# Optimization experiments

Measured on AMD Instinct MI355X. Metric: run time of the kernel, lower is better.

The kernel has to match this reference:

```python
import jax, jax.numpy as jnp
import numpy as np

NUM_CLASSES = 10
OUTPUT_DIM = 128
HIDDEN_DIM = 64


def setup_inputs() -> dict:
    key = jax.random.key(0)
    k1, k2, k3, k4, k5, k6 = jax.random.split(key, 6)
    B, S, F = 16, 4096, 512
    X_support = jax.random.normal(k1, (B, S, F), dtype=jnp.float32)
    y_support = jax.random.randint(k2, (B, S), 0, NUM_CLASSES, dtype=jnp.int32)
    # MLP params: Linear(6, HIDDEN) -> GELU -> Linear(HIDDEN, OUTPUT)
    w1 = jax.random.normal(k3, (6, HIDDEN_DIM), dtype=jnp.float32) * (1.0 / np.sqrt(6.0))
    b1 = jax.random.normal(k4, (HIDDEN_DIM,), dtype=jnp.float32) * 0.01
    w2 = jax.random.normal(k5, (HIDDEN_DIM, OUTPUT_DIM), dtype=jnp.float32) * (1.0 / np.sqrt(HIDDEN_DIM))
    b2 = jax.random.normal(k6, (OUTPUT_DIM,), dtype=jnp.float32) * 0.01
    return {"X_support": X_support, "y_support": y_support,
            "w1": w1, "b1": b1, "w2": w2, "b2": b2}


def _feature_target_stats(X, y):
    """Vectorized equivalent of FeatureTargetStatsEncoder per-(batch,feature) loops.
    X: [B, S, F] float, y: [B, S] int class labels. Returns stats [B, F, 6]."""
    B, S, F = X.shape
    missing_rate = jnp.isnan(X).astype(X.dtype).mean(axis=1)           # [B, F]
    Xc = jnp.nan_to_num(X, nan=0.0)
    gmean = Xc.mean(axis=1)                                            # [B, F]
    variance = Xc.var(axis=1)                                          # biased (unbiased=False)
    absX = jnp.abs(Xc)
    mean_abs = absX.mean(axis=1)
    max_abs = absX.max(axis=1)
    # unique_ratio: count distinct values per (b, f) via sort + diff
    xs = jnp.sort(Xc, axis=1)
    n_unique = 1.0 + (jnp.diff(xs, axis=1) != 0).astype(Xc.dtype).sum(axis=1)
    unique_ratio = n_unique / S
    # classification target score: between-class variance / overall variance
    onehot = jax.nn.one_hot(y, NUM_CLASSES, dtype=Xc.dtype)            # [B, S, C]
    counts = onehot.sum(axis=1)                                        # [B, C]
    csum = jnp.einsum('bsc,bsf->bcf', onehot, Xc)                      # [B, C, F]
    cmean = csum / jnp.maximum(counts, 1.0)[:, :, None]
    dev2 = (cmean - gmean[:, None, :]) ** 2
    between = (counts[:, :, None] * dev2).sum(axis=1) / jnp.maximum(counts.sum(axis=1), 1.0)[:, None]
    target_score = between / jnp.maximum(variance, 1e-6)
    stats = jnp.stack([target_score, missing_rate, unique_ratio,
                       variance, mean_abs, max_abs], axis=-1)          # [B, F, 6]
    return jnp.nan_to_num(stats, nan=0.0, posinf=0.0, neginf=0.0)


def reference(X_support, y_support, w1, b1, w2, b2):
    stats = _feature_target_stats(X_support, y_support)                # [B, F, 6]
    h = jax.nn.gelu(stats @ w1 + b1, approximate=False)               # exact GELU like nn.GELU()
    return h @ w2 + b2                                                 # [B, F, OUTPUT_DIM]
```

## Files before the change

kernel.cpp:

```cpp
#include <hip/hip_runtime.h>
#include <math.h>

#define NS 4096
#define NF 512
#define NB 16
#define NC 10
#define HSIZE 8192
#define HMASK 8191
#define HEMPTY 0xFFFFFFFFu
#define WS_XT_OFF 1024

__global__ void count_classes_kernel(const int* __restrict__ y, float* __restrict__ counts) {
    __shared__ int hist[NC];
    const int b = blockIdx.x;
    if (threadIdx.x < NC) hist[threadIdx.x] = 0;
    __syncthreads();
    for (int s = threadIdx.x; s < NS; s += blockDim.x)
        atomicAdd(&hist[y[b * NS + s]], 1);
    __syncthreads();
    if (threadIdx.x < NC) counts[b * NC + threadIdx.x] = (float)hist[threadIdx.x];
}

__device__ __forceinline__ float wave_reduce_add(float v) {
    #pragma unroll
    for (int off = 32; off > 0; off >>= 1) v += __shfl_down(v, off, 64);
    return v;
}
__device__ __forceinline__ float wave_reduce_max(float v) {
    #pragma unroll
    for (int off = 32; off > 0; off >>= 1) v = fmaxf(v, __shfl_down(v, off, 64));
    return v;
}

__launch_bounds__(256)
__global__ void transpose_kernel(const float* __restrict__ X, float* __restrict__ XT) {
    __shared__ float t[64][65];
    const int b  = blockIdx.x;
    const int s0 = blockIdx.y * 64;
    const int f0 = blockIdx.z * 64;
    const int tid = threadIdx.x;

    const int fi = (tid & 15) * 4;
    const int si = tid >> 4;
    const float* Xb = X + ((size_t)b * NS + s0) * NF + f0;
    #pragma unroll
    for (int i = 0; i < 4; i++) {
        const int s = si + 16 * i;
        const float4 v = *(const float4*)(Xb + (size_t)s * NF + fi);
        t[s][fi + 0] = v.x; t[s][fi + 1] = v.y;
        t[s][fi + 2] = v.z; t[s][fi + 3] = v.w;
    }
    __syncthreads();

    const int sj = (tid & 15) * 4;
    const int fj = tid >> 4;
    float* XTb = XT + ((size_t)b * NF + f0) * NS + s0;
    #pragma unroll
    for (int i = 0; i < 4; i++) {
        const int f = fj + 16 * i;
        float4 v;
        v.x = t[sj + 0][f]; v.y = t[sj + 1][f];
        v.z = t[sj + 2][f]; v.w = t[sj + 3][f];
        *(float4*)(XTb + (size_t)f * NS + sj) = v;
    }
}

__launch_bounds__(256)
__global__ void fused_stats_mlp_xt(const float* __restrict__ XT,
                                   const int* __restrict__ y,
                                   const float* __restrict__ counts,
                                   const float* __restrict__ w1,
                                   const float* __restrict__ b1,
                                   const float* __restrict__ w2,
                                   const float* __restrict__ b2,
                                   float* __restrict__ out) {
    __shared__ unsigned int hash[HSIZE];
    __shared__ float red[4][16];
    __shared__ float stats_s[6];
    __shared__ float h_s[64];

    const int w = blockIdx.x;
    const int g = (w & 7) * 1024 + (w >> 3);
    const int b = g >> 9;
    const int f = g & (NF - 1);
    const int tid = threadIdx.x;

    #pragma unroll
    for (int i = 0; i < HSIZE / 256; i++) hash[tid + i * 256] = HEMPTY;
    __syncthreads();

    const float4* Xc4 = (const float4*)(XT + ((size_t)b * NF + f) * NS);
    const int4*   yp4 = (const int4*)(y + (size_t)b * NS);

    float sum = 0.f, sumsq = 0.f, sumabs = 0.f, maxabs = 0.f, nancnt = 0.f, uniq = 0.f;
    float csum[NC];
    #pragma unroll
    for (int c = 0; c < NC; c++) csum[c] = 0.f;

    float4 xv[4]; int4 yv[4];
    #pragma unroll
    for (int k = 0; k < 4; k++) {
        xv[k] = Xc4[k * 256 + tid];
        yv[k] = yp4[k * 256 + tid];
    }

    #pragma unroll
    for (int k = 0; k < 4; k++) {
        const float xe[4] = { xv[k].x, xv[k].y, xv[k].z, xv[k].w };
        const int   ye[4] = { yv[k].x, yv[k].y, yv[k].z, yv[k].w };
        #pragma unroll
        for (int j = 0; j < 4; j++) {
            float x = xe[j];
            if (x != x) { nancnt += 1.f; x = 0.f; }
            sum += x;
            sumsq = fmaf(x, x, sumsq);
            const float a = fabsf(x);
            sumabs += a;
            maxabs = fmaxf(maxabs, a);
            const int yc = ye[j];
            #pragma unroll
            for (int c = 0; c < NC; c++) csum[c] += (yc == c) ? x : 0.f;
            unsigned int pat = __float_as_uint(x);
            if (pat == 0x80000000u) pat = 0u;
            unsigned int slot = (pat * 2654435761u) >> 19;
            for (;;) {
                const unsigned int old = atomicCAS(&hash[slot], HEMPTY, pat);
                if (old == HEMPTY) { uniq += 1.f; break; }
                if (old == pat) break;
                slot = (slot + 1) & HMASK;
            }
        }
    }

    sum    = wave_reduce_add(sum);
    sumsq  = wave_reduce_add(sumsq);
    sumabs = wave_reduce_add(sumabs);
    nancnt = wave_reduce_add(nancnt);
    uniq   = wave_reduce_add(uniq);
    maxabs = wave_reduce_max(maxabs);
    #pragma unroll
    for (int c = 0; c < NC; c++) csum[c] = wave_reduce_add(csum[c]);

    const int wave = tid >> 6, lane = tid & 63;
    if (lane == 0) {
        red[wave][0] = sum;    red[wave][1] = sumsq; red[wave][2] = sumabs;
        red[wave][3] = nancnt; red[wave][4] = uniq;  red[wave][5] = maxabs;
        #pragma unroll
        for (int c = 0; c < NC; c++) red[wave][6 + c] = csum[c];
    }
    __syncthreads();

    if (tid == 0) {
        float t[16];
        #pragma unroll
        for (int v = 0; v < 16; v++) t[v] = red[0][v];
        #pragma unroll
        for (int wv = 1; wv < 4; wv++) {
            #pragma unroll
            for (int v = 0; v < 16; v++) {
                if (v == 5) t[v] = fmaxf(t[v], red[wv][v]);
                else        t[v] += red[wv][v];
            }
        }
        const float invS = 1.f / (float)NS;
        const float gmean    = t[0] * invS;
        const float variance = fmaxf(t[1] * invS - gmean * gmean, 0.f);
        const float mean_abs = t[2] * invS;
        const float missing  = t[3] * invS;
        const float n_unique = t[4];
        const float max_abs  = t[5];
        float between = 0.f;
        #pragma unroll
        for (int c = 0; c < NC; c++) {
            const float cnt = counts[b * NC + c];
            const float cm  = t[6 + c] / fmaxf(cnt, 1.f);
            const float d   = cm - gmean;
            between += cnt * d * d;
        }
        between *= invS;
        const float target = between / fmaxf(variance, 1e-6f);
        float st[6] = { target, missing, n_unique * invS, variance, mean_abs, max_abs };
        #pragma unroll
        for (int i = 0; i < 6; i++) {
            float v = st[i];
            if (!(fabsf(v) < INFINITY)) v = 0.f;
            stats_s[i] = v;
        }
    }
    __syncthreads();

    if (tid < 64) {
        float z = b1[tid];
        #pragma unroll
        for (int i = 0; i < 6; i++) z = fmaf(stats_s[i], w1[i * 64 + tid], z);
        h_s[tid] = 0.5f * z * (1.f + erff(z * 0.70710678118654752440f));
    }
    __syncthreads();
    if (tid < 128) {
        float o = b2[tid];
        #pragma unroll
        for (int j = 0; j < 64; j++) o = fmaf(h_s[j], w2[j * 128 + tid], o);
        out[(size_t)g * 128 + tid] = o;
    }
}

__launch_bounds__(256)
__global__ void fused_stats_mlp_kernel(const float* __restrict__ X,
                                       const int* __restrict__ y,
                                       const float* __restrict__ counts,
                                       const float* __restrict__ w1,
                                       const float* __restrict__ b1,
                                       const float* __restrict__ w2,
                                       const float* __restrict__ b2,
                                       float* __restrict__ out) {
    __shared__ unsigned int hash[HSIZE];
    __shared__ float red[4][16];
    __shared__ float stats_s[6];
    __shared__ float h_s[64];

    const int w = blockIdx.x;
    const int g = (w & 7) * 1024 + (w >> 3);
    const int b = g >> 9;
    const int f = g & (NF - 1);
    const int tid = threadIdx.x;

    #pragma unroll
    for (int i = 0; i < HSIZE / 256; i++) hash[tid + i * 256] = HEMPTY;
    __syncthreads();

    const float* Xp = X + (size_t)b * NS * NF + f;
    const int*   yp = y + b * NS;

    float sum = 0.f, sumsq = 0.f, sumabs = 0.f, maxabs = 0.f, nancnt = 0.f, uniq = 0.f;
    float csum[NC];
    #pragma unroll
    for (int c = 0; c < NC; c++) csum[c] = 0.f;

    #pragma unroll
    for (int k0 = 0; k0 < 16; k0 += 8) {
        float xv[8]; int yv[8];
        #pragma unroll
        for (int k = 0; k < 8; k++) {
            const int s = (k0 + k) * 256 + tid;
            xv[k] = Xp[(size_t)s * NF];
            yv[k] = yp[s];
        }
        #pragma unroll
        for (int k = 0; k < 8; k++) {
            float x = xv[k];
            if (x != x) { nancnt += 1.f; x = 0.f; }
            sum += x;
            sumsq = fmaf(x, x, sumsq);
            const float a = fabsf(x);
            sumabs += a;
            maxabs = fmaxf(maxabs, a);
            const int yc = yv[k];
            #pragma unroll
            for (int c = 0; c < NC; c++) csum[c] += (yc == c) ? x : 0.f;
            unsigned int pat = __float_as_uint(x);
            if (pat == 0x80000000u) pat = 0u;
            unsigned int slot = (pat * 2654435761u) >> 19;
            for (;;) {
                const unsigned int old = atomicCAS(&hash[slot], HEMPTY, pat);
                if (old == HEMPTY) { uniq += 1.f; break; }
                if (old == pat) break;
                slot = (slot + 1) & HMASK;
            }
        }
    }

    sum    = wave_reduce_add(sum);
    sumsq  = wave_reduce_add(sumsq);
    sumabs = wave_reduce_add(sumabs);
    nancnt = wave_reduce_add(nancnt);
    uniq   = wave_reduce_add(uniq);
    maxabs = wave_reduce_max(maxabs);
    #pragma unroll
    for (int c = 0; c < NC; c++) csum[c] = wave_reduce_add(csum[c]);

    const int wave = tid >> 6, lane = tid & 63;
    if (lane == 0) {
        red[wave][0] = sum;    red[wave][1] = sumsq; red[wave][2] = sumabs;
        red[wave][3] = nancnt; red[wave][4] = uniq;  red[wave][5] = maxabs;
        #pragma unroll
        for (int c = 0; c < NC; c++) red[wave][6 + c] = csum[c];
    }
    __syncthreads();

    if (tid == 0) {
        float t[16];
        #pragma unroll
        for (int v = 0; v < 16; v++) t[v] = red[0][v];
        #pragma unroll
        for (int wv = 1; wv < 4; wv++) {
            #pragma unroll
            for (int v = 0; v < 16; v++) {
                if (v == 5) t[v] = fmaxf(t[v], red[wv][v]);
                else        t[v] += red[wv][v];
            }
        }
        const float invS = 1.f / (float)NS;
        const float gmean    = t[0] * invS;
        const float variance = fmaxf(t[1] * invS - gmean * gmean, 0.f);
        const float mean_abs = t[2] * invS;
        const float missing  = t[3] * invS;
        const float n_unique = t[4];
        const float max_abs  = t[5];
        float between = 0.f;
        #pragma unroll
        for (int c = 0; c < NC; c++) {
            const float cnt = counts[b * NC + c];
            const float cm  = t[6 + c] / fmaxf(cnt, 1.f);
            const float d   = cm - gmean;
            between += cnt * d * d;
        }
        between *= invS;
        const float target = between / fmaxf(variance, 1e-6f);
        float st[6] = { target, missing, n_unique * invS, variance, mean_abs, max_abs };
        #pragma unroll
        for (int i = 0; i < 6; i++) {
            float v = st[i];
            if (!(fabsf(v) < INFINITY)) v = 0.f;
            stats_s[i] = v;
        }
    }
    __syncthreads();

    if (tid < 64) {
        float z = b1[tid];
        #pragma unroll
        for (int i = 0; i < 6; i++) z = fmaf(stats_s[i], w1[i * 64 + tid], z);
        h_s[tid] = 0.5f * z * (1.f + erff(z * 0.70710678118654752440f));
    }
    __syncthreads();
    if (tid < 128) {
        float o = b2[tid];
        #pragma unroll
        for (int j = 0; j < 64; j++) o = fmaf(h_s[j], w2[j * 128 + tid], o);
        out[(size_t)g * 128 + tid] = o;
    }
}

extern "C" void kernel_launch(void* const* d_in, const int* in_sizes, int n_in,
                              void* d_out, int out_size, void* d_ws, size_t ws_size,
                              hipStream_t stream) {
    const float* X  = (const float*)d_in[0];
    const int*   y  = (const int*)d_in[1];
    const float* w1 = (const float*)d_in[2];
    const float* b1 = (const float*)d_in[3];
    const float* w2 = (const float*)d_in[4];
    const float* b2 = (const float*)d_in[5];
    float* out    = (float*)d_out;
    float* counts = (float*)d_ws;

    count_classes_kernel<<<NB, 256, 0, stream>>>(y, counts);

    const size_t xt_bytes = (size_t)NB * NF * NS * sizeof(float);
    if (ws_size >= xt_bytes + WS_XT_OFF) {
        float* XT = (float*)((char*)d_ws + WS_XT_OFF);
        transpose_kernel<<<dim3(NB, NS / 64, NF / 64), 256, 0, stream>>>(X, XT);
        fused_stats_mlp_xt<<<NB * NF, 256, 0, stream>>>(XT, y, counts, w1, b1, w2, b2, out);
    } else {
        fused_stats_mlp_kernel<<<NB * NF, 256, 0, stream>>>(X, y, counts, w1, b1, w2, b2, out);
    }
}
```

Before: 378.1 us.

## Software-pipeline hash-set CAS inserts and fold class counting into transpose

The unique-count hash insertion is split into a batched first CAS and a deferred collision-resolution step, interleaved with prefetch of the next X/y chunk so that LDS atomic latency overlaps with loads and arithmetic. The class histogram moves into the transpose kernel's first blocks, which removes one kernel launch. Reduction scratch now reuses the hash LDS buffer to cut shared memory, the hash reset uses vectorized stores, and launch bounds request 5 blocks per CU. This costs more registers, and the extra syncthreads inside a conditional branch of the transpose is uniform per block, so it is safe.

After: 388.5 us. 1.03x slower.

```diff
diff --git a/kernel.cpp b/kernel.cpp
--- a/kernel.cpp
+++ b/kernel.cpp
@@ -33,8 +33,10 @@
 }
 
 __launch_bounds__(256)
-__global__ void transpose_kernel(const float* __restrict__ X, float* __restrict__ XT) {
+__global__ void transpose_kernel(const float* __restrict__ X, float* __restrict__ XT,
+                                 const int* __restrict__ y, float* __restrict__ counts) {
     __shared__ float t[64][65];
+    __shared__ int hist[NC];
     const int b  = blockIdx.x;
     const int s0 = blockIdx.y * 64;
     const int f0 = blockIdx.z * 64;
@@ -63,9 +65,73 @@
         v.z = t[sj + 2][f]; v.w = t[sj + 3][f];
         *(float4*)(XTb + (size_t)f * NS + sj) = v;
     }
-}
-
-__launch_bounds__(256)
+
+    if (blockIdx.y == 0 && blockIdx.z == 0) {
+        if (tid < NC) hist[tid] = 0;
+        __syncthreads();
+        const int4* yb = (const int4*)(y + (size_t)b * NS);
+        #pragma unroll
+        for (int i = 0; i < 4; i++) {
+            const int4 v = yb[i * 256 + tid];
+            atomicAdd(&hist[v.x], 1); atomicAdd(&hist[v.y], 1);
+            atomicAdd(&hist[v.z], 1); atomicAdd(&hist[v.w], 1);
+        }
+        __syncthreads();
+        if (tid < NC) counts[b * NC + tid] = (float)hist[tid];
+    }
+}
+
+__device__ __forceinline__ void prep_group(const float4 xf, const int4 yi,
+    float& sum, float& sumsq, float& sumabs, float& maxabs, float& nancnt,
+    float* csum, unsigned int* P, unsigned int* S)
+{
+    const float xe[4] = { xf.x, xf.y, xf.z, xf.w };
+    const int   ye[4] = { yi.x, yi.y, yi.z, yi.w };
+    #pragma unroll
+    for (int j = 0; j < 4; j++) {
+        float x = xe[j];
+        if (x != x) { nancnt += 1.f; x = 0.f; }
+        sum += x;
+        sumsq = fmaf(x, x, sumsq);
+        const float a = fabsf(x);
+        sumabs += a;
+        maxabs = fmaxf(maxabs, a);
+        #pragma unroll
+        for (int c = 0; c < NC; c++) csum[c] += (ye[j] == c) ? x : 0.f;
+        unsigned int p = __float_as_uint(x);
+        if (p == 0x80000000u) p = 0u;
+        P[j] = p;
+        S[j] = (p * 2654435761u) >> 19;
+    }
+}
+
+__device__ __forceinline__ void cas_batch(unsigned int* hash,
+    const unsigned int* S, const unsigned int* P, unsigned int* O)
+{
+    #pragma unroll
+    for (int j = 0; j < 4; j++)
+        O[j] = atomicCAS(&hash[S[j]], HEMPTY, P[j]);
+}
+
+__device__ __forceinline__ void resolve_batch(unsigned int* hash,
+    const unsigned int* S, const unsigned int* P, const unsigned int* O, float& uniq)
+{
+    #pragma unroll
+    for (int j = 0; j < 4; j++) {
+        const unsigned int o = O[j];
+        if (o == HEMPTY) { uniq += 1.f; continue; }
+        if (o == P[j]) continue;
+        unsigned int sl = S[j];
+        for (;;) {
+            sl = (sl + 1) & HMASK;
+            const unsigned int oo = atomicCAS(&hash[sl], HEMPTY, P[j]);
+            if (oo == HEMPTY) { uniq += 1.f; break; }
+            if (oo == P[j]) break;
+        }
+    }
+}
+
+__launch_bounds__(256, 5)
 __global__ void fused_stats_mlp_xt(const float* __restrict__ XT,
                                    const int* __restrict__ y,
                                    const float* __restrict__ counts,
@@ -74,19 +140,19 @@
                                    const float* __restrict__ w2,
                                    const float* __restrict__ b2,
                                    float* __restrict__ out) {
-    __shared__ unsigned int hash[HSIZE];
-    __shared__ float red[4][16];
-    __shared__ float stats_s[6];
-    __shared__ float h_s[64];
+    __shared__ __align__(16) unsigned int hash[HSIZE];
 
     const int w = blockIdx.x;
     const int g = (w & 7) * 1024 + (w >> 3);
     const int b = g >> 9;
     const int f = g & (NF - 1);
     const int tid = threadIdx.x;
-
-    #pragma unroll
-    for (int i = 0; i < HSIZE / 256; i++) hash[tid + i * 256] = HEMPTY;
+    const int wave = tid >> 6, lane = tid & 63;
+
+    uint4* h4 = (uint4*)hash;
+    const uint4 e4 = make_uint4(HEMPTY, HEMPTY, HEMPTY, HEMPTY);
+    #pragma unroll
+    for (int i = 0; i < HSIZE / 4 / 256; i++) h4[i * 256 + tid] = e4;
     __syncthreads();
 
     const float4* Xc4 = (const float4*)(XT + ((size_t)b * NF + f) * NS);
@@ -97,40 +163,34 @@
     #pragma unroll
     for (int c = 0; c < NC; c++) csum[c] = 0.f;
 
-    float4 xv[4]; int4 yv[4];
-    #pragma unroll
-    for (int k = 0; k < 4; k++) {
-        xv[k] = Xc4[k * 256 + tid];
-        yv[k] = yp4[k * 256 + tid];
-    }
-
-    #pragma unroll
-    for (int k = 0; k < 4; k++) {
-        const float xe[4] = { xv[k].x, xv[k].y, xv[k].z, xv[k].w };
-        const int   ye[4] = { yv[k].x, yv[k].y, yv[k].z, yv[k].w };
-        #pragma unroll
-        for (int j = 0; j < 4; j++) {
-            float x = xe[j];
-            if (x != x) { nancnt += 1.f; x = 0.f; }
-            sum += x;
-            sumsq = fmaf(x, x, sumsq);
-            const float a = fabsf(x);
-            sumabs += a;
-            maxabs = fmaxf(maxabs, a);
-            const int yc = ye[j];
-            #pragma unroll
-            for (int c = 0; c < NC; c++) csum[c] += (yc == c) ? x : 0.f;
-            unsigned int pat = __float_as_uint(x);
-            if (pat == 0x80000000u) pat = 0u;
-            unsigned int slot = (pat * 2654435761u) >> 19;
-            for (;;) {
-                const unsigned int old = atomicCAS(&hash[slot], HEMPTY, pat);
-                if (old == HEMPTY) { uniq += 1.f; break; }
-                if (old == pat) break;
-                slot = (slot + 1) & HMASK;
-            }
-        }
-    }
+    unsigned int PA[4], SA[4], OA[4], PB[4], SB[4], OB[4];
+
+    float4 xc = Xc4[tid];              int4 yc = yp4[tid];
+    float4 xn = Xc4[256 + tid];        int4 yn = yp4[256 + tid];
+
+    prep_group(xc, yc, sum, sumsq, sumabs, maxabs, nancnt, csum, PA, SA);
+    cas_batch(hash, SA, PA, OA);
+    xc = xn; yc = yn;
+    xn = Xc4[512 + tid]; yn = yp4[512 + tid];
+    prep_group(xc, yc, sum, sumsq, sumabs, maxabs, nancnt, csum, PB, SB);
+    cas_batch(hash, SB, PB, OB);
+    resolve_batch(hash, SA, PA, OA, uniq);
+    xc = xn; yc = yn;
+    xn = Xc4[768 + tid]; yn = yp4[768 + tid];
+    prep_group(xc, yc, sum, sumsq, sumabs, maxabs, nancnt, csum, PA, SA);
+    cas_batch(hash, SA, PA, OA);
+    resolve_batch(hash, SB, PB, OB, uniq);
+    xc = xn; yc = yn;
+    prep_group(xc, yc, sum, sumsq, sumabs, maxabs, nancnt, csum, PB, SB);
+    cas_batch(hash, SB, PB, OB);
+    resolve_batch(hash, SA, PA, OA, uniq);
+    resolve_batch(hash, SB, PB, OB, uniq);
+
+    __syncthreads();
+
+    float (*red)[16] = (float(*)[16])hash;
+    float* stats_s   = (float*)hash + 64;
+    float* h_s       = (float*)hash + 128;
 
     sum    = wave_reduce_add(sum);
     sumsq  = wave_reduce_add(sumsq);
@@ -141,7 +201,6 @@
     #pragma unroll
     for (int c = 0; c < NC; c++) csum[c] = wave_reduce_add(csum[c]);
 
-    const int wave = tid >> 6, lane = tid & 63;
     if (lane == 0) {
         red[wave][0] = sum;    red[wave][1] = sumsq; red[wave][2] = sumabs;
         red[wave][3] = nancnt; red[wave][4] = uniq;  red[wave][5] = maxabs;
@@ -353,14 +412,13 @@
     float* out    = (float*)d_out;
     float* counts = (float*)d_ws;
 
-    count_classes_kernel<<<NB, 256, 0, stream>>>(y, counts);
-
     const size_t xt_bytes = (size_t)NB * NF * NS * sizeof(float);
     if (ws_size >= xt_bytes + WS_XT_OFF) {
         float* XT = (float*)((char*)d_ws + WS_XT_OFF);
-        transpose_kernel<<<dim3(NB, NS / 64, NF / 64), 256, 0, stream>>>(X, XT);
+        transpose_kernel<<<dim3(NB, NS / 64, NF / 64), 256, 0, stream>>>(X, XT, y, counts);
         fused_stats_mlp_xt<<<NB * NF, 256, 0, stream>>>(XT, y, counts, w1, b1, w2, b2, out);
     } else {
+        count_classes_kernel<<<NB, 256, 0, stream>>>(y, counts);
         fused_stats_mlp_kernel<<<NB * NF, 256, 0, stream>>>(X, y, counts, w1, b1, w2, b2, out);
     }
 }
```

## Fold class counting into transpose and widen stats blocks to 512 threads

Applied to the files above, without the earlier changes.

Class histogram computation moves into the first block of each batch in the transpose kernel, which removes one kernel launch. The fused stats kernel now runs 512 threads per block, so each thread handles 8 samples instead of 16. It clears the hash table with 128-bit stores and reuses the hash shared memory for the reduction scratch after a barrier, which lowers the LDS footprint. The costs are more wave-level reductions per block, extra barriers, and possibly more contention on the hash-table atomics.

Result: slower. 388.7 us (+2.8%).

```diff
diff --git a/kernel.cpp b/kernel.cpp
--- a/kernel.cpp
+++ b/kernel.cpp
@@ -33,8 +33,10 @@
 }
 
 __launch_bounds__(256)
-__global__ void transpose_kernel(const float* __restrict__ X, float* __restrict__ XT) {
+__global__ void transpose_kernel(const float* __restrict__ X, float* __restrict__ XT,
+                                 const int* __restrict__ y, float* __restrict__ counts) {
     __shared__ float t[64][65];
+    __shared__ int hist[NC];
     const int b  = blockIdx.x;
     const int s0 = blockIdx.y * 64;
     const int f0 = blockIdx.z * 64;
@@ -63,9 +65,23 @@
         v.z = t[sj + 2][f]; v.w = t[sj + 3][f];
         *(float4*)(XTb + (size_t)f * NS + sj) = v;
     }
-}
-
-__launch_bounds__(256)
+
+    if (blockIdx.y == 0 && blockIdx.z == 0) {
+        if (tid < NC) hist[tid] = 0;
+        __syncthreads();
+        const int4* yb = (const int4*)(y + (size_t)b * NS);
+        #pragma unroll
+        for (int i = 0; i < 4; i++) {
+            const int4 v = yb[i * 256 + tid];
+            atomicAdd(&hist[v.x], 1); atomicAdd(&hist[v.y], 1);
+            atomicAdd(&hist[v.z], 1); atomicAdd(&hist[v.w], 1);
+        }
+        __syncthreads();
+        if (tid < NC) counts[b * NC + tid] = (float)hist[tid];
+    }
+}
+
+__launch_bounds__(512, 8)
 __global__ void fused_stats_mlp_xt(const float* __restrict__ XT,
                                    const int* __restrict__ y,
                                    const float* __restrict__ counts,
@@ -74,19 +90,19 @@
                                    const float* __restrict__ w2,
                                    const float* __restrict__ b2,
                                    float* __restrict__ out) {
-    __shared__ unsigned int hash[HSIZE];
-    __shared__ float red[4][16];
-    __shared__ float stats_s[6];
-    __shared__ float h_s[64];
+    __shared__ __align__(16) unsigned int hash[HSIZE];
 
     const int w = blockIdx.x;
     const int g = (w & 7) * 1024 + (w >> 3);
     const int b = g >> 9;
     const int f = g & (NF - 1);
     const int tid = threadIdx.x;
-
-    #pragma unroll
-    for (int i = 0; i < HSIZE / 256; i++) hash[tid + i * 256] = HEMPTY;
+    const int wave = tid >> 6, lane = tid & 63;
+
+    uint4* h4 = (uint4*)hash;
+    const uint4 e4 = make_uint4(HEMPTY, HEMPTY, HEMPTY, HEMPTY);
+    #pragma unroll
+    for (int i = 0; i < HSIZE / 4 / 512; i++) h4[i * 512 + tid] = e4;
     __syncthreads();
 
     const float4* Xc4 = (const float4*)(XT + ((size_t)b * NF + f) * NS);
@@ -97,15 +113,15 @@
     #pragma unroll
     for (int c = 0; c < NC; c++) csum[c] = 0.f;
 
-    float4 xv[4]; int4 yv[4];
-    #pragma unroll
-    for (int k = 0; k < 4; k++) {
-        xv[k] = Xc4[k * 256 + tid];
-        yv[k] = yp4[k * 256 + tid];
-    }
-
-    #pragma unroll
-    for (int k = 0; k < 4; k++) {
+    float4 xv[2]; int4 yv[2];
+    #pragma unroll
+    for (int k = 0; k < 2; k++) {
+        xv[k] = Xc4[k * 512 + tid];
+        yv[k] = yp4[k * 512 + tid];
+    }
+
+    #pragma unroll
+    for (int k = 0; k < 2; k++) {
         const float xe[4] = { xv[k].x, xv[k].y, xv[k].z, xv[k].w };
         const int   ye[4] = { yv[k].x, yv[k].y, yv[k].z, yv[k].w };
         #pragma unroll
@@ -132,6 +148,12 @@
         }
     }
 
+    __syncthreads();
+
+    float (*red)[16] = (float(*)[16])hash;
+    float* stats_s   = (float*)hash + 128;
+    float* h_s       = (float*)hash + 192;
+
     sum    = wave_reduce_add(sum);
     sumsq  = wave_reduce_add(sumsq);
     sumabs = wave_reduce_add(sumabs);
@@ -141,7 +163,6 @@
     #pragma unroll
     for (int c = 0; c < NC; c++) csum[c] = wave_reduce_add(csum[c]);
 
-    const int wave = tid >> 6, lane = tid & 63;
     if (lane == 0) {
         red[wave][0] = sum;    red[wave][1] = sumsq; red[wave][2] = sumabs;
         red[wave][3] = nancnt; red[wave][4] = uniq;  red[wave][5] = maxabs;
@@ -155,7 +176,7 @@
         #pragma unroll
         for (int v = 0; v < 16; v++) t[v] = red[0][v];
         #pragma unroll
-        for (int wv = 1; wv < 4; wv++) {
+        for (int wv = 1; wv < 8; wv++) {
             #pragma unroll
             for (int v = 0; v < 16; v++) {
                 if (v == 5) t[v] = fmaxf(t[v], red[wv][v]);
@@ -353,14 +374,13 @@
     float* out    = (float*)d_out;
     float* counts = (float*)d_ws;
 
-    count_classes_kernel<<<NB, 256, 0, stream>>>(y, counts);
-
     const size_t xt_bytes = (size_t)NB * NF * NS * sizeof(float);
     if (ws_size >= xt_bytes + WS_XT_OFF) {
         float* XT = (float*)((char*)d_ws + WS_XT_OFF);
-        transpose_kernel<<<dim3(NB, NS / 64, NF / 64), 256, 0, stream>>>(X, XT);
-        fused_stats_mlp_xt<<<NB * NF, 256, 0, stream>>>(XT, y, counts, w1, b1, w2, b2, out);
+        transpose_kernel<<<dim3(NB, NS / 64, NF / 64), 256, 0, stream>>>(X, XT, y, counts);
+        fused_stats_mlp_xt<<<NB * NF, 512, 0, stream>>>(XT, y, counts, w1, b1, w2, b2, out);
     } else {
+        count_classes_kernel<<<NB, 256, 0, stream>>>(y, counts);
         fused_stats_mlp_kernel<<<NB * NF, 256, 0, stream>>>(X, y, counts, w1, b1, w2, b2, out);
     }
 }
```
